# Optimization experiments

Hardware: AMD Instinct MI355X
Metric: run time of the kernel (lower is better)

## Reference

```python
import jax, jax.numpy as jnp
import numpy as np


def setup_inputs() -> dict:
    key = jax.random.key(0)
    ks = jax.random.split(key, 6)
    B, H, KVH, D = 8, 32, 8, 128
    PAGES_PER_SEQ, PAGE_SIZE, L_MAX = 512, 16, 4096
    total_pages = B * PAGES_PER_SEQ  # 4096
    kv_len = PAGES_PER_SEQ * PAGE_SIZE  # 8192 tokens per sequence
    q = jax.random.normal(ks[0], (B, H, 1, D), dtype=jnp.float32)
    paged_kv_cache = jax.random.normal(ks[1], (total_pages, 2, KVH, PAGE_SIZE, D), dtype=jnp.float32)
    kv_page_indptr = (jnp.arange(B + 1, dtype=jnp.int32) * PAGES_PER_SEQ)
    kv_page_indices = jax.random.permutation(ks[2], total_pages).astype(jnp.int32)
    sparse_ind = jax.random.randint(ks[3], (B, H, L_MAX), 0, kv_len, dtype=jnp.int32)
    sparse_nnz = jax.random.randint(ks[4], (B, H), 1, L_MAX + 1, dtype=jnp.int32)
    return {
        "q": q,
        "paged_kv_cache": paged_kv_cache,
        "kv_page_indptr": kv_page_indptr,
        "kv_page_indices": kv_page_indices,
        "sparse_ind": sparse_ind,
        "sparse_nnz": sparse_nnz,
    }


def reference(q, paged_kv_cache, kv_page_indptr, kv_page_indices, sparse_ind, sparse_nnz):
    # q: [B, H, 1, D]; paged_kv_cache: [P, 2, KVH, PS, D]
    B, H, _, D = q.shape
    KVH, PS = paged_kv_cache.shape[2], paged_kv_cache.shape[3]
    groups = H // KVH
    L = sparse_ind.shape[-1]
    scale = jnp.float32(1.0 / (D ** 0.5))

    # Paged-table lookup: token index -> (logical page, offset) -> physical page id
    page_idx = sparse_ind // PS               # [B, H, L]
    off_in_page = sparse_ind % PS             # [B, H, L]
    page_id = kv_page_indices[kv_page_indptr[:B][:, None, None] + page_idx]  # [B, H, L]

    kv_head = (jnp.arange(H) // groups)[None, :, None]  # GQA head mapping, [1, H, 1]
    K = paged_kv_cache[page_id, 0, kv_head, off_in_page]  # [B, H, L, D]
    V = paged_kv_cache[page_id, 1, kv_head, off_in_page]  # [B, H, L, D]

    qk = jnp.einsum("bhd,bhld->bhl", q[:, :, 0, :], K)
    mask = jnp.arange(L)[None, None, :] < sparse_nnz[:, :, None]
    # Kernel uses additive -1e6 for masked lanes (K loaded as 0 -> qk==0)
    scores = jnp.where(mask, qk * scale, jnp.float32(-1e6))
    p = jax.nn.softmax(scores, axis=-1)       # online-softmax is math-equivalent
    out = jnp.einsum("bhl,bhld->bhd", p, V)
    return out[:, :, None, :]                  # [B, H, 1, D]
```

## Files before the change

kernel.cpp:

```cpp
#include <hip/hip_runtime.h>
#include <math.h>

#define BB   8
#define HH   32
#define KVHH 8
#define DD   128
#define PSZ  16
#define LMAX 4096
#define CHUNK 256
#define NCHUNK (LMAX / CHUNK)

#define PAGE_STRIDE (2 * KVHH * PSZ * DD)
#define KV_OFFSET   (KVHH * PSZ * DD)
#define HEAD_STRIDE (PSZ * DD)

__global__ __launch_bounds__(256) void attn_partial(
    const float* __restrict__ q,
    const float* __restrict__ cache,
    const int*   __restrict__ indptr,
    const int*   __restrict__ pageind,
    const int*   __restrict__ sind,
    const int*   __restrict__ snnz,
    float* __restrict__ ws_m,
    float* __restrict__ ws_l,
    float* __restrict__ ws_acc)
{
    const int blk   = blockIdx.x;
    const int chunk = blk % NCHUNK;
    const int bh    = blk / NCHUNK;
    const int b     = bh / HH;
    const int h     = bh % HH;
    const int kvh   = h >> 2;
    const int tid   = threadIdx.x;

    const int nnz = snnz[bh];
    const int l0  = chunk * CHUNK;
    const int widx = bh * NCHUNK + chunk;

    if (l0 >= nnz) {
        if (tid == 0) { ws_m[widx] = -1e30f; ws_l[widx] = 0.0f; }
        if (tid < DD) ws_acc[widx * DD + tid] = 0.0f;
        return;
    }
    const int nrows = min(nnz - l0, CHUNK);

    __shared__ unsigned int s_base[CHUNK];
    __shared__ float s_m[8], s_l[8];
    __shared__ float s_acc[8][DD];

    const int indbase = indptr[b];
    const int* si = sind + bh * LMAX + l0;
    if (tid < nrows) {
        const int idx  = si[tid];
        const int pidx = idx >> 4;
        const int off  = idx & 15;
        const int pid  = pageind[indbase + pidx];
        s_base[tid] = (unsigned)pid * PAGE_STRIDE
                    + (unsigned)(kvh * HEAD_STRIDE + off * DD);
    }
    __syncthreads();

    const int lane32 = tid & 31;
    const int hw     = tid >> 5;

    const float4 q4 = *(const float4*)(q + bh * DD + lane32 * 4);
    const float cscale = 0.08838834764831845f * 1.4426950408889634f;

    float  m0 = -1e30f, l0s = 0.0f;
    float  m1 = -1e30f, l1s = 0.0f;
    float4 a0 = make_float4(0.f, 0.f, 0.f, 0.f);
    float4 a1 = make_float4(0.f, 0.f, 0.f, 0.f);

    for (int i = hw; i < nrows; i += 16) {
        const bool has1 = (i + 8) < nrows;
        const unsigned b0 = s_base[i];
        const unsigned b1 = s_base[has1 ? (i + 8) : i];

        const float* kp0 = cache + b0 + lane32 * 4;
        const float* kp1 = cache + b1 + lane32 * 4;
        const float4 k0 = *(const float4*)kp0;
        const float4 v0 = *(const float4*)(kp0 + KV_OFFSET);
        const float4 k1 = *(const float4*)kp1;
        const float4 v1 = *(const float4*)(kp1 + KV_OFFSET);

        float s0 = k0.x * q4.x + k0.y * q4.y + k0.z * q4.z + k0.w * q4.w;
        float s1 = k1.x * q4.x + k1.y * q4.y + k1.z * q4.z + k1.w * q4.w;
        s0 += __shfl_xor(s0, 16);  s1 += __shfl_xor(s1, 16);
        s0 += __shfl_xor(s0, 8);   s1 += __shfl_xor(s1, 8);
        s0 += __shfl_xor(s0, 4);   s1 += __shfl_xor(s1, 4);
        s0 += __shfl_xor(s0, 2);   s1 += __shfl_xor(s1, 2);
        s0 += __shfl_xor(s0, 1);   s1 += __shfl_xor(s1, 1);

        {
            const float t    = s0 * cscale;
            const float mn   = fmaxf(m0, t);
            const float corr = exp2f(m0 - mn);
            const float p    = exp2f(t - mn);
            l0s = l0s * corr + p;
            a0.x = a0.x * corr + p * v0.x;
            a0.y = a0.y * corr + p * v0.y;
            a0.z = a0.z * corr + p * v0.z;
            a0.w = a0.w * corr + p * v0.w;
            m0 = mn;
        }
        if (has1) {
            const float t    = s1 * cscale;
            const float mn   = fmaxf(m1, t);
            const float corr = exp2f(m1 - mn);
            const float p    = exp2f(t - mn);
            l1s = l1s * corr + p;
            a1.x = a1.x * corr + p * v1.x;
            a1.y = a1.y * corr + p * v1.y;
            a1.z = a1.z * corr + p * v1.z;
            a1.w = a1.w * corr + p * v1.w;
            m1 = mn;
        }
    }

    {
        const float mn = fmaxf(m0, m1);
        const float f0 = exp2f(m0 - mn);
        const float f1 = exp2f(m1 - mn);
        l0s = l0s * f0 + l1s * f1;
        a0.x = a0.x * f0 + a1.x * f1;
        a0.y = a0.y * f0 + a1.y * f1;
        a0.z = a0.z * f0 + a1.z * f1;
        a0.w = a0.w * f0 + a1.w * f1;
        m0 = mn;
    }

    if (lane32 == 0) { s_m[hw] = m0; s_l[hw] = l0s; }
    *(float4*)&s_acc[hw][lane32 * 4] = a0;
    __syncthreads();

    if (tid < DD) {
        float M = s_m[0];
        #pragma unroll
        for (int i = 1; i < 8; i++) M = fmaxf(M, s_m[i]);
        float tot = 0.f, a = 0.f;
        #pragma unroll
        for (int i = 0; i < 8; i++) {
            const float f = exp2f(s_m[i] - M);
            tot += s_l[i] * f;
            a   += s_acc[i][tid] * f;
        }
        ws_acc[widx * DD + tid] = a;
        if (tid == 0) { ws_m[widx] = M; ws_l[widx] = tot; }
    }
}

__global__ __launch_bounds__(128) void attn_combine(
    const float* __restrict__ ws_m,
    const float* __restrict__ ws_l,
    const float* __restrict__ ws_acc,
    float* __restrict__ out)
{
    const int bh = blockIdx.x;
    const int d  = threadIdx.x;

    float M = -1e30f;
    #pragma unroll
    for (int i = 0; i < NCHUNK; i++) M = fmaxf(M, ws_m[bh * NCHUNK + i]);

    float tot = 0.f, a = 0.f;
    #pragma unroll
    for (int i = 0; i < NCHUNK; i++) {
        const float f = exp2f(ws_m[bh * NCHUNK + i] - M);
        tot += ws_l[bh * NCHUNK + i] * f;
        a   += ws_acc[(bh * NCHUNK + i) * DD + d] * f;
    }
    out[bh * DD + d] = a / tot;
}

extern "C" void kernel_launch(void* const* d_in, const int* in_sizes, int n_in,
                              void* d_out, int out_size, void* d_ws, size_t ws_size,
                              hipStream_t stream) {
    const float* q      = (const float*)d_in[0];
    const float* cache  = (const float*)d_in[1];
    const int*   indptr = (const int*)d_in[2];
    const int*   pgind  = (const int*)d_in[3];
    const int*   sind   = (const int*)d_in[4];
    const int*   snnz   = (const int*)d_in[5];
    float* out = (float*)d_out;

    float* ws_m   = (float*)d_ws;
    float* ws_l   = ws_m + BB * HH * NCHUNK;
    float* ws_acc = ws_l + BB * HH * NCHUNK;

    attn_partial<<<dim3(BB * HH * NCHUNK), dim3(256), 0, stream>>>(
        q, cache, indptr, pgind, sind, snnz, ws_m, ws_l, ws_acc);
    attn_combine<<<dim3(BB * HH), dim3(128), 0, stream>>>(
        ws_m, ws_l, ws_acc, out);
}
```

Before: 681.7 us.

## Remap blocks per XCD by KV head and split scoring from PV accumulation

Block indices are remapped so that all chunks of the four query heads sharing a KV head (same batch) land on the same XCD, which should improve L2 reuse of the gathered K/V rows across the GQA group. The per-row online softmax is replaced with a two-phase scheme: scores are computed four rows at a time and stored in shared memory, a block-wide max and sum reduction follows, and then a second pass loads V and accumulates with the final probabilities. This removes the per-row exp2 rescaling and the merge step and raises memory-level parallelism, at the cost of extra barriers and a separate V-load pass.

```diff
diff --git a/kernel.cpp b/kernel.cpp
--- a/kernel.cpp
+++ b/kernel.cpp
@@ -26,15 +26,19 @@
     float* __restrict__ ws_acc)
 {
     const int blk   = blockIdx.x;
-    const int chunk = blk % NCHUNK;
-    const int bh    = blk / NCHUNK;
-    const int b     = bh / HH;
-    const int h     = bh % HH;
-    const int kvh   = h >> 2;
+    const int xcd   = blk & 7;
+    const int slot  = (blk >> 3) & 63;
+    const int super = blk >> 9;
+    const int g     = super * 8 + xcd;
+    const int b     = g >> 3;
+    const int kvh   = g & 7;
+    const int h     = (kvh << 2) + (slot >> 4);
+    const int chunk = slot & 15;
+    const int bh    = b * HH + h;
     const int tid   = threadIdx.x;
 
-    const int nnz = snnz[bh];
-    const int l0  = chunk * CHUNK;
+    const int nnz  = snnz[bh];
+    const int l0   = chunk * CHUNK;
     const int widx = bh * NCHUNK + chunk;
 
     if (l0 >= nnz) {
@@ -43,109 +47,109 @@
         return;
     }
     const int nrows = min(nnz - l0, CHUNK);
+    const int nr32  = (nrows + 31) & ~31;
 
-    __shared__ unsigned int s_base[CHUNK];
-    __shared__ float s_m[8], s_l[8];
-    __shared__ float s_acc[8][DD];
+    __shared__ unsigned s_base[CHUNK];
+    __shared__ float    s_p[CHUNK];
+    __shared__ float    s_red[16];
+    __shared__ float    s_acc[8][DD];
 
     const int indbase = indptr[b];
     const int* si = sind + bh * LMAX + l0;
-    if (tid < nrows) {
-        const int idx  = si[tid];
-        const int pidx = idx >> 4;
-        const int off  = idx & 15;
-        const int pid  = pageind[indbase + pidx];
-        s_base[tid] = (unsigned)pid * PAGE_STRIDE
-                    + (unsigned)(kvh * HEAD_STRIDE + off * DD);
+    {
+        unsigned base = 0u;
+        if (tid < nrows) {
+            const int idx = si[tid];
+            const int pid = pageind[indbase + (idx >> 4)];
+            base = (unsigned)pid * PAGE_STRIDE
+                 + (unsigned)(kvh * HEAD_STRIDE + (idx & 15) * DD);
+        }
+        s_base[tid] = base;
     }
     __syncthreads();
 
     const int lane32 = tid & 31;
     const int hw     = tid >> 5;
-
-    const float4 q4 = *(const float4*)(q + bh * DD + lane32 * 4);
+    const float4 q4  = *(const float4*)(q + bh * DD + lane32 * 4);
     const float cscale = 0.08838834764831845f * 1.4426950408889634f;
 
-    float  m0 = -1e30f, l0s = 0.0f;
-    float  m1 = -1e30f, l1s = 0.0f;
-    float4 a0 = make_float4(0.f, 0.f, 0.f, 0.f);
-    float4 a1 = make_float4(0.f, 0.f, 0.f, 0.f);
-
-    for (int i = hw; i < nrows; i += 16) {
-        const bool has1 = (i + 8) < nrows;
+    for (int i = hw; i < nr32; i += 32) {
         const unsigned b0 = s_base[i];
-        const unsigned b1 = s_base[has1 ? (i + 8) : i];
-
-        const float* kp0 = cache + b0 + lane32 * 4;
-        const float* kp1 = cache + b1 + lane32 * 4;
-        const float4 k0 = *(const float4*)kp0;
-        const float4 v0 = *(const float4*)(kp0 + KV_OFFSET);
-        const float4 k1 = *(const float4*)kp1;
-        const float4 v1 = *(const float4*)(kp1 + KV_OFFSET);
-
-        float s0 = k0.x * q4.x + k0.y * q4.y + k0.z * q4.z + k0.w * q4.w;
-        float s1 = k1.x * q4.x + k1.y * q4.y + k1.z * q4.z + k1.w * q4.w;
-        s0 += __shfl_xor(s0, 16);  s1 += __shfl_xor(s1, 16);
-        s0 += __shfl_xor(s0, 8);   s1 += __shfl_xor(s1, 8);
-        s0 += __shfl_xor(s0, 4);   s1 += __shfl_xor(s1, 4);
-        s0 += __shfl_xor(s0, 2);   s1 += __shfl_xor(s1, 2);
-        s0 += __shfl_xor(s0, 1);   s1 += __shfl_xor(s1, 1);
-
-        {
-            const float t    = s0 * cscale;
-            const float mn   = fmaxf(m0, t);
-            const float corr = exp2f(m0 - mn);
-            const float p    = exp2f(t - mn);
-            l0s = l0s * corr + p;
-            a0.x = a0.x * corr + p * v0.x;
-            a0.y = a0.y * corr + p * v0.y;
-            a0.z = a0.z * corr + p * v0.z;
-            a0.w = a0.w * corr + p * v0.w;
-            m0 = mn;
+        const unsigned b1 = s_base[i + 8];
+        const unsigned b2 = s_base[i + 16];
+        const unsigned b3 = s_base[i + 24];
+        const float4 k0 = *(const float4*)(cache + b0 + lane32 * 4);
+        const float4 k1 = *(const float4*)(cache + b1 + lane32 * 4);
+        const float4 k2 = *(const float4*)(cache + b2 + lane32 * 4);
+        const float4 k3 = *(const float4*)(cache + b3 + lane32 * 4);
+        float s0 = k0.x*q4.x + k0.y*q4.y + k0.z*q4.z + k0.w*q4.w;
+        float s1 = k1.x*q4.x + k1.y*q4.y + k1.z*q4.z + k1.w*q4.w;
+        float s2 = k2.x*q4.x + k2.y*q4.y + k2.z*q4.z + k2.w*q4.w;
+        float s3 = k3.x*q4.x + k3.y*q4.y + k3.z*q4.z + k3.w*q4.w;
+        #pragma unroll
+        for (int m = 16; m >= 1; m >>= 1) {
+            s0 += __shfl_xor(s0, m);
+            s1 += __shfl_xor(s1, m);
+            s2 += __shfl_xor(s2, m);
+            s3 += __shfl_xor(s3, m);
         }
-        if (has1) {
-            const float t    = s1 * cscale;
-            const float mn   = fmaxf(m1, t);
-            const float corr = exp2f(m1 - mn);
-            const float p    = exp2f(t - mn);
-            l1s = l1s * corr + p;
-            a1.x = a1.x * corr + p * v1.x;
-            a1.y = a1.y * corr + p * v1.y;
-            a1.z = a1.z * corr + p * v1.z;
-            a1.w = a1.w * corr + p * v1.w;
-            m1 = mn;
+        if (lane32 == 0) {
+            s_p[i]      = (i      < nrows) ? s0 * cscale : -1e30f;
+            s_p[i + 8]  = (i + 8  < nrows) ? s1 * cscale : -1e30f;
+            s_p[i + 16] = (i + 16 < nrows) ? s2 * cscale : -1e30f;
+            s_p[i + 24] = (i + 24 < nrows) ? s3 * cscale : -1e30f;
         }
     }
+    __syncthreads();
 
-    {
-        const float mn = fmaxf(m0, m1);
-        const float f0 = exp2f(m0 - mn);
-        const float f1 = exp2f(m1 - mn);
-        l0s = l0s * f0 + l1s * f1;
-        a0.x = a0.x * f0 + a1.x * f1;
-        a0.y = a0.y * f0 + a1.y * f1;
-        a0.z = a0.z * f0 + a1.z * f1;
-        a0.w = a0.w * f0 + a1.w * f1;
-        m0 = mn;
+    const float sc = (tid < nr32) ? s_p[tid] : -1e30f;
+    float wm = sc;
+    #pragma unroll
+    for (int m = 32; m >= 1; m >>= 1) wm = fmaxf(wm, __shfl_xor(wm, m));
+    const int wv = tid >> 6;
+    if ((tid & 63) == 0) s_red[wv] = wm;
+    __syncthreads();
+    const float M = fmaxf(fmaxf(s_red[0], s_red[1]), fmaxf(s_red[2], s_red[3]));
+    const float p = (tid < nr32) ? exp2f(sc - M) : 0.0f;
+    if (tid < nr32) s_p[tid] = p;
+    float wl = p;
+    #pragma unroll
+    for (int m = 32; m >= 1; m >>= 1) wl += __shfl_xor(wl, m);
+    if ((tid & 63) == 0) s_red[8 + wv] = wl;
+    __syncthreads();
+
+    float4 acc = make_float4(0.f, 0.f, 0.f, 0.f);
+    for (int i = hw; i < nr32; i += 32) {
+        const unsigned b0 = s_base[i];
+        const unsigned b1 = s_base[i + 8];
+        const unsigned b2 = s_base[i + 16];
+        const unsigned b3 = s_base[i + 24];
+        const float p0 = s_p[i];
+        const float p1 = s_p[i + 8];
+        const float p2 = s_p[i + 16];
+        const float p3 = s_p[i + 24];
+        const float4 v0 = *(const float4*)(cache + b0 + KV_OFFSET + lane32 * 4);
+        const float4 v1 = *(const float4*)(cache + b1 + KV_OFFSET + lane32 * 4);
+        const float4 v2 = *(const float4*)(cache + b2 + KV_OFFSET + lane32 * 4);
+        const float4 v3 = *(const float4*)(cache + b3 + KV_OFFSET + lane32 * 4);
+        acc.x += p0*v0.x; acc.y += p0*v0.y; acc.z += p0*v0.z; acc.w += p0*v0.w;
+        acc.x += p1*v1.x; acc.y += p1*v1.y; acc.z += p1*v1.z; acc.w += p1*v1.w;
+        acc.x += p2*v2.x; acc.y += p2*v2.y; acc.z += p2*v2.z; acc.w += p2*v2.w;
+        acc.x += p3*v3.x; acc.y += p3*v3.y; acc.z += p3*v3.z; acc.w += p3*v3.w;
     }
 
-    if (lane32 == 0) { s_m[hw] = m0; s_l[hw] = l0s; }
-    *(float4*)&s_acc[hw][lane32 * 4] = a0;
+    *(float4*)&s_acc[hw][lane32 * 4] = acc;
     __syncthreads();
 
     if (tid < DD) {
-        float M = s_m[0];
+        float a = 0.f;
         #pragma unroll
-        for (int i = 1; i < 8; i++) M = fmaxf(M, s_m[i]);
-        float tot = 0.f, a = 0.f;
-        #pragma unroll
-        for (int i = 0; i < 8; i++) {
-            const float f = exp2f(s_m[i] - M);
-            tot += s_l[i] * f;
-            a   += s_acc[i][tid] * f;
+        for (int i = 0; i < 8; i++) a += s_acc[i][tid];
+        ws_acc[widx * DD + tid] = a;
+        if (tid == 0) {
+            ws_m[widx] = M;
+            ws_l[widx] = s_red[8] + s_red[9] + s_red[10] + s_red[11];
         }
-        ws_acc[widx * DD + tid] = a;
-        if (tid == 0) { ws_m[widx] = M; ws_l[widx] = tot; }
     }
 }
 
```

After: 666.1 us. 2.3% less time.
